# Performance work log

Measured on AMD Instinct MI355X. Metric: run time of the kernel, lower is better.

Reference implementation:

```python
import jax, jax.numpy as jnp
import numpy as np

E, EDIM, NDIM, H = 262144, 256, 256, 8
DH = NDIM // H
EPS = 1e-5  # torch nn.LayerNorm default


def _param(k, shape, scale=0.02):
    return jax.random.normal(k, shape, jnp.float32) * scale


def setup_inputs() -> dict:
    key = jax.random.key(0)
    ks = jax.random.split(key, 12)
    return {
        "x": jax.random.normal(ks[0], (E, EDIM), jnp.float32),
        "src_x": jax.random.normal(ks[1], (E, NDIM), jnp.float32),
        "dst_x": jax.random.normal(ks[2], (E, NDIM), jnp.float32),
        # multi-head cross-attention params (q from edge feats, k/v from node feats)
        "Wq": _param(ks[3], (EDIM, NDIM)), "bq": jnp.zeros((NDIM,), jnp.float32),
        "Wk": _param(ks[4], (NDIM, NDIM)), "bk": jnp.zeros((NDIM,), jnp.float32),
        "Wv": _param(ks[5], (NDIM, NDIM)), "bv": jnp.zeros((NDIM,), jnp.float32),
        "Wo": _param(ks[6], (NDIM, EDIM)), "bo": jnp.zeros((EDIM,), jnp.float32),
        "W1": _param(ks[7], (EDIM, 4 * EDIM)), "b1": jnp.zeros((4 * EDIM,), jnp.float32),
        "W2": _param(ks[8], (4 * EDIM, EDIM)), "b2": jnp.zeros((EDIM,), jnp.float32),
        # two LayerNorms
        "g1": jnp.ones((EDIM,), jnp.float32), "be1": jnp.zeros((EDIM,), jnp.float32),
        "g2": jnp.ones((EDIM,), jnp.float32), "be2": jnp.zeros((EDIM,), jnp.float32),
    }


def _layer_norm(h, g, b):
    m = jnp.mean(h, axis=-1, keepdims=True)
    v = jnp.mean(jnp.square(h - m), axis=-1, keepdims=True)
    return (h - m) * jax.lax.rsqrt(v + EPS) * g + b


def reference(x, src_x, dst_x, Wq, bq, Wk, bk, Wv, bv, Wo, bo,
              W1, b1, W2, b2, g1, be1, g2, be2):
    # per-edge cross-attention: query = edge feat (len 1), keys/values = (src, dst) (len 2)
    q = (x @ Wq + bq).reshape(E, H, DH)                 # [E,H,DH]
    kv = jnp.stack([src_x, dst_x], axis=1)              # [E,2,NDIM]
    k = (kv @ Wk + bk).reshape(E, 2, H, DH)
    v = (kv @ Wv + bv).reshape(E, 2, H, DH)
    scale = 1.0 / float(np.sqrt(DH))
    scores = jnp.einsum('ehd,ekhd->ehk', q, k) * scale  # [E,H,2]
    attn = jax.nn.softmax(scores, axis=-1)
    ctx = jnp.einsum('ehk,ekhd->ehd', attn, v).reshape(E, NDIM)
    out = ctx @ Wo + bo                                  # [E,EDIM]
    h = _layer_norm(x + out, g1, be1)
    ff = jax.nn.relu(h @ W1 + b1) @ W2 + b2
    return _layer_norm(h + ff, g2, be2)
```

## Files before the change

kernel.cpp:

```cpp
#include <hip/hip_runtime.h>
#include <hip/hip_bf16.h>
#include <math.h>

#define NROWS   262144
#define ABM     64
#define FBM     128
#define ATHR    256
#define FTHR    512
#define LDSB_A  (32768 + 32768 + 2048 + 512)
#define LDSB_B  (65536 + 65536)

using bf16x8 = __attribute__((ext_vector_type(8))) short;
using s16x4  = __attribute__((ext_vector_type(4))) short;
using f32x4  = __attribute__((ext_vector_type(4))) float;

__device__ __forceinline__ short f2bf(float f) {
  __hip_bfloat16 h = __float2bfloat16(f);
  return __builtin_bit_cast(short, h);
}
__device__ __forceinline__ float bf2f(short s) {
  __hip_bfloat16 h = __builtin_bit_cast(__hip_bfloat16, s);
  return __bfloat162float(h);
}
__device__ __forceinline__ unsigned pack2(float a, float b) {
  return (unsigned)(unsigned short)f2bf(a) | ((unsigned)(unsigned short)f2bf(b) << 16);
}
template <int RSTR>
__device__ __forceinline__ int swzR(int row, int col) {
  return row * RSTR + ((col * 2) ^ ((row & 7) << 4));
}
__device__ __forceinline__ int swz(int row, int col) {
  return swzR<512>(row, col);
}

__device__ __forceinline__ float red16(float p) {
  p += __shfl_xor(p, 1, 64);
  p += __shfl_xor(p, 2, 64);
  p += __shfl_xor(p, 4, 64);
  p += __shfl_xor(p, 8, 64);
  return p;
}

template <int MF, int NF, int KLEN = 256, int RSTR = 512>
__device__ __forceinline__ void gemmA(const char* __restrict__ Abuf,
                                      const short* __restrict__ WT, int Kw,
                                      int col0, int koff, int li, int hi,
                                      f32x4 (&acc)[MF][NF]) {
  const short* wp[NF];
#pragma unroll
  for (int n = 0; n < NF; ++n)
    wp[n] = WT + (size_t)(col0 + 16 * n + li) * Kw + koff + hi * 8;
#pragma unroll 2
  for (int kk = 0; kk < KLEN; kk += 32) {
    int ka = kk + hi * 8;
    bf16x8 b[NF];
#pragma unroll
    for (int n = 0; n < NF; ++n) b[n] = *(const bf16x8*)(wp[n] + kk);
    bf16x8 a[MF];
#pragma unroll
    for (int m = 0; m < MF; ++m)
      a[m] = *(const bf16x8*)(Abuf + swzR<RSTR>(16 * m + li, ka));
#pragma unroll
    for (int m = 0; m < MF; ++m)
#pragma unroll
      for (int n = 0; n < NF; ++n)
        acc[m][n] = __builtin_amdgcn_mfma_f32_16x16x32_bf16(a[m], b[n], acc[m][n], 0, 0, 0);
  }
}

template <int MF, int NF, int KLEN = 256, int RSTR = 512>
__device__ __forceinline__ void gemmF(const char* __restrict__ Abuf,
                                      const short* __restrict__ WT, int Kw,
                                      int col0, int koff, int li, int hi,
                                      f32x4 (&acc)[MF][NF]) {
  const short* wp[NF];
#pragma unroll
  for (int n = 0; n < NF; ++n)
    wp[n] = WT + (size_t)(col0 + 16 * n + li) * Kw + koff + hi * 8;
#pragma unroll 2
  for (int kk = 0; kk < KLEN; kk += 32) {
    int ka = kk + hi * 8;
    bf16x8 b[NF];
#pragma unroll
    for (int n = 0; n < NF; ++n) b[n] = *(const bf16x8*)(wp[n] + kk);
    bf16x8 a[MF];
#pragma unroll
    for (int m = 0; m < MF; ++m)
      a[m] = *(const bf16x8*)(Abuf + swzR<RSTR>(16 * m + li, ka));
#pragma unroll
    for (int m = 0; m < MF; ++m)
#pragma unroll
      for (int n = 0; n < NF; ++n)
        acc[m][n] = __builtin_amdgcn_mfma_f32_16x16x32_bf16(a[m], b[n], acc[m][n], 0, 0, 0);
  }
}

__device__ __forceinline__ void stage8(float4 (&ld)[8],
                                       const float* __restrict__ g,
                                       int tid, int half) {
#pragma unroll
  for (int it = 0; it < 8; ++it) {
    int idx = (half * 8 + it) * ATHR + tid;
    ld[it] = *(const float4*)(g + (idx >> 6) * 256 + ((idx & 63) << 2));
  }
}
__device__ __forceinline__ void write8(float4 (&ld)[8],
                                       char* __restrict__ buf,
                                       int tid, int half) {
#pragma unroll
  for (int it = 0; it < 8; ++it) {
    int idx = (half * 8 + it) * ATHR + tid;
    int r = idx >> 6, c = (idx & 63) << 2;
    s16x4 o;
    o[0] = f2bf(ld[it].x); o[1] = f2bf(ld[it].y);
    o[2] = f2bf(ld[it].z); o[3] = f2bf(ld[it].w);
    *(s16x4*)(buf + swz(r, c)) = o;
  }
}

__global__ void prep(const float* __restrict__ Wq, const float* __restrict__ Wk,
                     const float* __restrict__ Wv, const float* __restrict__ Wo,
                     const float* __restrict__ W1, const float* __restrict__ W2,
                     short* __restrict__ wt) {
  int idx = blockIdx.x * blockDim.x + threadIdx.x;
  if (idx < 262144) {
    int m = idx >> 16;
    const float* W = (m == 0) ? Wq : (m == 1) ? Wk : (m == 2) ? Wv : Wo;
    float s = (m == 0) ? 0.17677669529663687f : 1.0f;
    int l = idx & 65535;
    int n = l >> 8, k = l & 255;
    wt[idx] = f2bf(W[k * 256 + n] * s);
  } else if (idx < 524288) {
    int l = idx - 262144;
    int n = l >> 8, k = l & 255;
    wt[idx] = f2bf(W1[k * 1024 + n]);
  } else {
    int l = idx - 524288;
    int n = l >> 10, k = l & 1023;
    wt[idx] = f2bf(W2[k * 256 + n]);
  }
}

__global__ __launch_bounds__(ATHR, 2)
void attn_ln1(const float* __restrict__ x, const float* __restrict__ sx,
              const float* __restrict__ dx,
              const float* __restrict__ bq, const float* __restrict__ bv,
              const float* __restrict__ bo,
              const float* __restrict__ g1, const float* __restrict__ be1,
              const short* __restrict__ wt, short* __restrict__ hout) {
  extern __shared__ char sm[];
  char*  Cbuf = sm;
  char*  Tbuf = sm + 32768;
  float* sc   = (float*)(sm + 65536);
  float* scrM = (float*)(sm + 67584);

  const short* WqT = wt;
  const short* WkT = wt + 65536;
  const short* WvT = wt + 131072;
  const short* WoT = wt + 196608;

  const int tid  = threadIdx.x;
  const int w    = tid >> 6;
  const int lane = tid & 63;
  const int li   = lane & 15;
  const int hi   = lane >> 4;
  const int cw   = w * 64;
  const size_t row0 = (size_t)blockIdx.x * ABM;

  const float* xt = x  + row0 * 256;
  const float* st = sx + row0 * 256;
  const float* dt = dx + row0 * 256;

  float4 ld[8];

  stage8(ld, xt, tid, 0);
  write8(ld, Cbuf, tid, 0);
  stage8(ld, xt, tid, 1);
  write8(ld, Cbuf, tid, 1);
  __syncthreads();

  unsigned qb[4][4][2];
  {
    f32x4 qa[4][4];
#pragma unroll
    for (int m = 0; m < 4; ++m)
#pragma unroll
      for (int n = 0; n < 4; ++n) qa[m][n] = (f32x4){0.f, 0.f, 0.f, 0.f};
    stage8(ld, dt, tid, 0);
    gemmA<4, 4, 128>(Cbuf, WqT, 256, cw, 0, li, hi, qa);
    write8(ld, Tbuf, tid, 0);
    stage8(ld, dt, tid, 1);
    gemmA<4, 4, 128>(Cbuf + 256, WqT, 256, cw, 128, li, hi, qa);
    write8(ld, Tbuf, tid, 1);
    const float scl = 0.17677669529663687f;
#pragma unroll
    for (int n = 0; n < 4; ++n) {
      float bqn = bq[cw + 16 * n + li] * scl;
#pragma unroll
      for (int m = 0; m < 4; ++m) {
        qb[m][n][0] = pack2(qa[m][n][0] + bqn, qa[m][n][1] + bqn);
        qb[m][n][1] = pack2(qa[m][n][2] + bqn, qa[m][n][3] + bqn);
      }
    }
  }
  __syncthreads();

#define QF(m, n, j) bf2f((short)(((j) & 1) ? (qb[m][n][(j) >> 1] >> 16) \
                                           : (qb[m][n][(j) >> 1] & 0xffffu)))

  f32x4 vd[4][4];
  {
    stage8(ld, st, tid, 0);
#pragma unroll
    for (int hh = 0; hh < 2; ++hh) {
      f32x4 ka[4][2];
#pragma unroll
      for (int m = 0; m < 4; ++m)
#pragma unroll
        for (int n = 0; n < 2; ++n) ka[m][n] = (f32x4){0.f, 0.f, 0.f, 0.f};
      gemmA<4, 2>(Tbuf, WkT, 256, cw + 32 * hh, 0, li, hi, ka);
#pragma unroll
      for (int m = 0; m < 4; ++m)
#pragma unroll
        for (int j = 0; j < 4; ++j) {
          float pr = red16(QF(m, 2 * hh, j) * ka[m][0][j] +
                           QF(m, 2 * hh + 1, j) * ka[m][1][j]);
          if (li == 0) sc[(w * 2 + hh) * 64 + 16 * m + 4 * hi + j] = pr;
        }
    }
#pragma unroll
    for (int m = 0; m < 4; ++m)
#pragma unroll
      for (int n = 0; n < 4; ++n) vd[m][n] = (f32x4){0.f, 0.f, 0.f, 0.f};
    gemmA<4, 4>(Tbuf, WvT, 256, cw, 0, li, hi, vd);
  }
  __syncthreads();
  write8(ld, Tbuf, tid, 0);
  stage8(ld, st, tid, 1);
  write8(ld, Tbuf, tid, 1);
  __syncthreads();

#pragma unroll
  for (int hh = 0; hh < 2; ++hh) {
    f32x4 ka[4][2];
#pragma unroll
    for (int m = 0; m < 4; ++m)
#pragma unroll
      for (int n = 0; n < 2; ++n) ka[m][n] = (f32x4){0.f, 0.f, 0.f, 0.f};
    gemmA<4, 2>(Tbuf, WkT, 256, cw + 32 * hh, 0, li, hi, ka);
#pragma unroll
    for (int m = 0; m < 4; ++m)
#pragma unroll
      for (int j = 0; j < 4; ++j) {
        float ps = red16(QF(m, 2 * hh, j) * ka[m][0][j] +
                         QF(m, 2 * hh + 1, j) * ka[m][1][j]);
        int r = 16 * m + 4 * hi + j;
        float pdv = sc[(w * 2 + hh) * 64 + r];
        float awv = 1.f / (1.f + expf(pdv - ps));
        if (li == 0) sc[(w * 2 + hh) * 64 + r] = awv;
      }
  }
  {
    f32x4 vs[4][4];
#pragma unroll
    for (int m = 0; m < 4; ++m)
#pragma unroll
      for (int n = 0; n < 4; ++n) vs[m][n] = (f32x4){0.f, 0.f, 0.f, 0.f};
    gemmA<4, 4>(Tbuf, WvT, 256, cw, 0, li, hi, vs);
#pragma unroll
    for (int hh = 0; hh < 2; ++hh)
#pragma unroll
      for (int n2 = 0; n2 < 2; ++n2) {
        int n = 2 * hh + n2;
        float bvn = bv[cw + 16 * n + li];
#pragma unroll
        for (int m = 0; m < 4; ++m)
#pragma unroll
          for (int j = 0; j < 4; ++j) {
            float a = sc[(w * 2 + hh) * 64 + 16 * m + 4 * hi + j];
            vs[m][n][j] = a * vs[m][n][j] + (1.f - a) * vd[m][n][j] + bvn;
          }
      }
    __syncthreads();
#pragma unroll
    for (int m = 0; m < 4; ++m)
#pragma unroll
      for (int n = 0; n < 4; ++n)
#pragma unroll
        for (int j = 0; j < 4; ++j)
          *(short*)(Tbuf + swz(16 * m + 4 * hi + j, cw + 16 * n + li)) = f2bf(vs[m][n][j]);
  }
  __syncthreads();

  {
    f32x4 oa[4][4];
#pragma unroll
    for (int m = 0; m < 4; ++m)
#pragma unroll
      for (int n = 0; n < 4; ++n) oa[m][n] = (f32x4){0.f, 0.f, 0.f, 0.f};
    gemmA<4, 4>(Tbuf, WoT, 256, cw, 0, li, hi, oa);
#pragma unroll
    for (int n = 0; n < 4; ++n) {
      float bon = bo[cw + 16 * n + li];
#pragma unroll
      for (int m = 0; m < 4; ++m)
#pragma unroll
        for (int j = 0; j < 4; ++j) {
          int r = 16 * m + 4 * hi + j;
          float xv = bf2f(*(short*)(Cbuf + swz(r, cw + 16 * n + li)));
          oa[m][n][j] += bon + xv;
        }
    }
#pragma unroll
    for (int m = 0; m < 4; ++m)
#pragma unroll
      for (int j = 0; j < 4; ++j) {
        int r = 16 * m + 4 * hi + j;
        float sv = oa[m][0][j] + oa[m][1][j] + oa[m][2][j] + oa[m][3][j];
        float qv = oa[m][0][j] * oa[m][0][j] + oa[m][1][j] * oa[m][1][j]
                 + oa[m][2][j] * oa[m][2][j] + oa[m][3][j] * oa[m][3][j];
        float s = red16(sv);
        float q = red16(qv);
        if (li == 0) { sc[(w * 64 + r) * 2] = s; sc[(w * 64 + r) * 2 + 1] = q; }
      }
    __syncthreads();
    if (tid < ABM) {
      float S = 0.f, Q = 0.f;
#pragma unroll
      for (int ww = 0; ww < 4; ++ww) {
        S += sc[(ww * 64 + tid) * 2];
        Q += sc[(ww * 64 + tid) * 2 + 1];
      }
      float mean = S * (1.f / 256.f);
      float var  = Q * (1.f / 256.f) - mean * mean;
      scrM[tid * 2] = mean;
      scrM[tid * 2 + 1] = rsqrtf(var + 1e-5f);
    }
    __syncthreads();
#pragma unroll
    for (int n = 0; n < 4; ++n) {
      float g1n = g1[cw + 16 * n + li];
      float b1n = be1[cw + 16 * n + li];
#pragma unroll
      for (int m = 0; m < 4; ++m)
#pragma unroll
        for (int j = 0; j < 4; ++j) {
          int r = 16 * m + 4 * hi + j;
          float mean = scrM[r * 2], rs = scrM[r * 2 + 1];
          *(short*)(Cbuf + swz(r, cw + 16 * n + li)) =
              f2bf((oa[m][n][j] - mean) * rs * g1n + b1n);
        }
    }
  }
  __syncthreads();

  {
    short* hrow = hout + row0 * 256;
#pragma unroll
    for (int t = 0; t < 8; ++t) {
      int idx = t * ATHR + tid;
      int r = idx >> 5, c16 = idx & 31;
      bf16x8 v = *(bf16x8*)(Cbuf + r * 512 + ((c16 * 16) ^ ((r & 7) << 4)));
      *(bf16x8*)(hrow + r * 256 + c16 * 8) = v;
    }
  }
#undef QF
}

__global__ __launch_bounds__(FTHR, 2)
void ffn_ln2(const short* __restrict__ hin, const float* __restrict__ b1,
             const float* __restrict__ b2,
             const float* __restrict__ g2, const float* __restrict__ be2,
             const short* __restrict__ wt, float* __restrict__ out) {
  extern __shared__ char sm[];
  char* Cbuf = sm;
  char* Hbuf = sm + 65536;
  float* scrP = (float*)Hbuf;
  float* scrM = (float*)(Hbuf + 8192);

  const short* W1T = wt + 262144;
  const short* W2T = wt + 524288;

  const int tid  = threadIdx.x;
  const int w    = tid >> 6;
  const int lane = tid & 63;
  const int li   = lane & 15;
  const int hi   = lane >> 4;
  const int cw   = w * 32;
  const size_t row0 = (size_t)blockIdx.x * FBM;

  {
    const short* hrow = hin + row0 * 256;
#pragma unroll
    for (int t = 0; t < 8; ++t) {
      int idx = t * FTHR + tid;
      int r = idx >> 5, c16 = idx & 31;
      bf16x8 v = *(const bf16x8*)(hrow + r * 256 + c16 * 8);
      *(bf16x8*)(Cbuf + r * 512 + ((c16 * 16) ^ ((r & 7) << 4))) = v;
    }
  }
  __syncthreads();

  f32x4 a2[8][2];
#pragma unroll
  for (int m = 0; m < 8; ++m)
#pragma unroll
    for (int n = 0; n < 2; ++n) a2[m][n] = (f32x4){0.f, 0.f, 0.f, 0.f};
#pragma unroll 1
  for (int c = 0; c < 4; ++c) {
#pragma unroll
    for (int nf = 0; nf < 2; ++nf) {
      f32x4 a1[8][1];
#pragma unroll
      for (int m = 0; m < 8; ++m) a1[m][0] = (f32x4){0.f, 0.f, 0.f, 0.f};
      gemmF<8, 1, 256, 512>(Cbuf, W1T, 256, 256 * c + cw + 16 * nf, 0, li, hi, a1);
      float b1n = b1[256 * c + cw + 16 * nf + li];
      int lc = cw + 16 * nf + li;
#pragma unroll
      for (int m = 0; m < 8; ++m)
#pragma unroll
        for (int j = 0; j < 4; ++j) {
          int r = 16 * m + 4 * hi + j;
          *(short*)(Hbuf + swzR<512>(r, lc)) = f2bf(fmaxf(a1[m][0][j] + b1n, 0.f));
        }
    }
    __syncthreads();
    gemmF<8, 2, 256, 512>(Hbuf, W2T, 1024, cw, 256 * c, li, hi, a2);
    __syncthreads();
  }

  {
#pragma unroll
    for (int n = 0; n < 2; ++n) {
      float b2n = b2[cw + 16 * n + li];
#pragma unroll
      for (int m = 0; m < 8; ++m)
#pragma unroll
        for (int j = 0; j < 4; ++j) {
          int r = 16 * m + 4 * hi + j;
          a2[m][n][j] += b2n + bf2f(*(short*)(Cbuf + swz(r, cw + 16 * n + li)));
        }
    }
  }
  __syncthreads();

#pragma unroll
  for (int m = 0; m < 8; ++m)
#pragma unroll
    for (int j = 0; j < 4; ++j) {
      int r = 16 * m + 4 * hi + j;
      float sv = a2[m][0][j] + a2[m][1][j];
      float qv = a2[m][0][j] * a2[m][0][j] + a2[m][1][j] * a2[m][1][j];
      float s = red16(sv);
      float q = red16(qv);
      if (li == 0) { scrP[(w * 128 + r) * 2] = s; scrP[(w * 128 + r) * 2 + 1] = q; }
    }
  __syncthreads();
  if (tid < FBM) {
    float S = 0.f, Q = 0.f;
#pragma unroll
    for (int ww = 0; ww < 8; ++ww) {
      S += scrP[(ww * 128 + tid) * 2];
      Q += scrP[(ww * 128 + tid) * 2 + 1];
    }
    float mean = S * (1.f / 256.f);
    float var  = Q * (1.f / 256.f) - mean * mean;
    scrM[tid * 2] = mean;
    scrM[tid * 2 + 1] = rsqrtf(var + 1e-5f);
  }
  __syncthreads();

  {
    float g2n[2], b2n[2];
#pragma unroll
    for (int n = 0; n < 2; ++n) {
      g2n[n] = g2[cw + 16 * n + li];
      b2n[n] = be2[cw + 16 * n + li];
    }
    float* orow = out + row0 * 256;
#pragma unroll
    for (int hf = 0; hf < 4; ++hf) {
#pragma unroll
      for (int m2 = 0; m2 < 2; ++m2) {
        int m = 2 * hf + m2;
#pragma unroll
        for (int n = 0; n < 2; ++n)
#pragma unroll
          for (int j = 0; j < 4; ++j) {
            int r = 16 * m + 4 * hi + j;
            float mean = scrM[r * 2], rs = scrM[r * 2 + 1];
            int rr = r - 32 * hf;
            *(float*)(Cbuf + rr * 1024 + (((cw + 16 * n + li) * 4) ^ ((rr & 7) << 4)))
                = (a2[m][n][j] - mean) * rs * g2n[n] + b2n[n];
          }
      }
      __syncthreads();
#pragma unroll
      for (int t = 0; t < 4; ++t) {
        int idx = t * FTHR + tid;
        int r = idx >> 6, c4 = idx & 63;
        f32x4 v = *(f32x4*)(Cbuf + r * 1024 + ((c4 * 16) ^ ((r & 7) << 4)));
        *(f32x4*)(orow + (hf * 32 + r) * 256 + c4 * 4) = v;
      }
      __syncthreads();
    }
  }
}

extern "C" void kernel_launch(void* const* d_in, const int* in_sizes, int n_in,
                              void* d_out, int out_size, void* d_ws, size_t ws_size,
                              hipStream_t stream) {
  const float* x   = (const float*)d_in[0];
  const float* sx  = (const float*)d_in[1];
  const float* dx  = (const float*)d_in[2];
  const float* Wq  = (const float*)d_in[3];
  const float* bq  = (const float*)d_in[4];
  const float* Wk  = (const float*)d_in[5];
  const float* Wv  = (const float*)d_in[7];
  const float* bv  = (const float*)d_in[8];
  const float* Wo  = (const float*)d_in[9];
  const float* bo  = (const float*)d_in[10];
  const float* W1  = (const float*)d_in[11];
  const float* b1  = (const float*)d_in[12];
  const float* W2  = (const float*)d_in[13];
  const float* b2  = (const float*)d_in[14];
  const float* g1  = (const float*)d_in[15];
  const float* be1 = (const float*)d_in[16];
  const float* g2  = (const float*)d_in[17];
  const float* be2 = (const float*)d_in[18];
  short* wt = (short*)d_ws;
  short* hbuf = wt + 786432;

  prep<<<dim3(1536), dim3(512), 0, stream>>>(Wq, Wk, Wv, Wo, W1, W2, wt);
  attn_ln1<<<dim3(NROWS / ABM), dim3(ATHR), LDSB_A, stream>>>(
      x, sx, dx, bq, bv, bo, g1, be1, wt, hbuf);
  ffn_ln2<<<dim3(NROWS / FBM), dim3(FTHR), LDSB_B, stream>>>(
      hbuf, b1, b2, g2, be2, wt, (float*)d_out);
}
```

Baseline: 1.075 ms.

## Double FFN block threads to 1024 with 16 waves each owning 16 columns

The FFN+LayerNorm kernel now launches 1024 threads per block instead of 512, so each of 16 waves owns a 16-column slice rather than 32. Per-thread accumulators halve, and the load, LN partial-sum and store loops are resized to match. The aim is more waves in flight to hide memory and MFMA latency. The cost is that each wave reloads the full A-operand from LDS for narrower outputs, LDS traffic per MFMA doubles, the LN reduction gets twice as many partials, and block-wide barriers cover more waves.

```diff
diff --git a/kernel.cpp b/kernel.cpp
--- a/kernel.cpp
+++ b/kernel.cpp
@@ -6,7 +6,7 @@
 #define ABM     64
 #define FBM     128
 #define ATHR    256
-#define FTHR    512
+#define FTHR    1024
 #define LDSB_A  (32768 + 32768 + 2048 + 512)
 #define LDSB_B  (65536 + 65536)
 
@@ -367,7 +367,7 @@
 #undef QF
 }
 
-__global__ __launch_bounds__(FTHR, 2)
+__global__ __launch_bounds__(FTHR, 4)
 void ffn_ln2(const short* __restrict__ hin, const float* __restrict__ b1,
              const float* __restrict__ b2,
              const float* __restrict__ g2, const float* __restrict__ be2,
@@ -376,7 +376,7 @@
   char* Cbuf = sm;
   char* Hbuf = sm + 65536;
   float* scrP = (float*)Hbuf;
-  float* scrM = (float*)(Hbuf + 8192);
+  float* scrM = (float*)(Hbuf + 16384);
 
   const short* W1T = wt + 262144;
   const short* W2T = wt + 524288;
@@ -386,13 +386,13 @@
   const int lane = tid & 63;
   const int li   = lane & 15;
   const int hi   = lane >> 4;
-  const int cw   = w * 32;
+  const int cw   = w * 16;
   const size_t row0 = (size_t)blockIdx.x * FBM;
 
   {
     const short* hrow = hin + row0 * 256;
 #pragma unroll
-    for (int t = 0; t < 8; ++t) {
+    for (int t = 0; t < 4; ++t) {
       int idx = t * FTHR + tid;
       int r = idx >> 5, c16 = idx & 31;
       bf16x8 v = *(const bf16x8*)(hrow + r * 256 + c16 * 8);
@@ -401,21 +401,18 @@
   }
   __syncthreads();
 
-  f32x4 a2[8][2];
-#pragma unroll
-  for (int m = 0; m < 8; ++m)
-#pragma unroll
-    for (int n = 0; n < 2; ++n) a2[m][n] = (f32x4){0.f, 0.f, 0.f, 0.f};
+  f32x4 a2[8][1];
+#pragma unroll
+  for (int m = 0; m < 8; ++m) a2[m][0] = (f32x4){0.f, 0.f, 0.f, 0.f};
 #pragma unroll 1
   for (int c = 0; c < 4; ++c) {
-#pragma unroll
-    for (int nf = 0; nf < 2; ++nf) {
-      f32x4 a1[8][1];
-#pragma unroll
-      for (int m = 0; m < 8; ++m) a1[m][0] = (f32x4){0.f, 0.f, 0.f, 0.f};
-      gemmF<8, 1, 256, 512>(Cbuf, W1T, 256, 256 * c + cw + 16 * nf, 0, li, hi, a1);
-      float b1n = b1[256 * c + cw + 16 * nf + li];
-      int lc = cw + 16 * nf + li;
+    f32x4 a1[8][1];
+#pragma unroll
+    for (int m = 0; m < 8; ++m) a1[m][0] = (f32x4){0.f, 0.f, 0.f, 0.f};
+    gemmF<8, 1, 256, 512>(Cbuf, W1T, 256, 256 * c + cw, 0, li, hi, a1);
+    {
+      float b1n = b1[256 * c + cw + li];
+      int lc = cw + li;
 #pragma unroll
       for (int m = 0; m < 8; ++m)
 #pragma unroll
@@ -425,22 +422,19 @@
         }
     }
     __syncthreads();
-    gemmF<8, 2, 256, 512>(Hbuf, W2T, 1024, cw, 256 * c, li, hi, a2);
+    gemmF<8, 1, 256, 512>(Hbuf, W2T, 1024, cw, 256 * c, li, hi, a2);
     __syncthreads();
   }
 
   {
-#pragma unroll
-    for (int n = 0; n < 2; ++n) {
-      float b2n = b2[cw + 16 * n + li];
-#pragma unroll
-      for (int m = 0; m < 8; ++m)
-#pragma unroll
-        for (int j = 0; j < 4; ++j) {
-          int r = 16 * m + 4 * hi + j;
-          a2[m][n][j] += b2n + bf2f(*(short*)(Cbuf + swz(r, cw + 16 * n + li)));
-        }
-    }
+    float b2n = b2[cw + li];
+#pragma unroll
+    for (int m = 0; m < 8; ++m)
+#pragma unroll
+      for (int j = 0; j < 4; ++j) {
+        int r = 16 * m + 4 * hi + j;
+        a2[m][0][j] += b2n + bf2f(*(short*)(Cbuf + swz(r, cw + li)));
+      }
   }
   __syncthreads();
 
@@ -449,17 +443,15 @@
 #pragma unroll
     for (int j = 0; j < 4; ++j) {
       int r = 16 * m + 4 * hi + j;
-      float sv = a2[m][0][j] + a2[m][1][j];
-      float qv = a2[m][0][j] * a2[m][0][j] + a2[m][1][j] * a2[m][1][j];
-      float s = red16(sv);
-      float q = red16(qv);
+      float s = red16(a2[m][0][j]);
+      float q = red16(a2[m][0][j] * a2[m][0][j]);
       if (li == 0) { scrP[(w * 128 + r) * 2] = s; scrP[(w * 128 + r) * 2 + 1] = q; }
     }
   __syncthreads();
   if (tid < FBM) {
     float S = 0.f, Q = 0.f;
 #pragma unroll
-    for (int ww = 0; ww < 8; ++ww) {
+    for (int ww = 0; ww < 16; ++ww) {
       S += scrP[(ww * 128 + tid) * 2];
       Q += scrP[(ww * 128 + tid) * 2 + 1];
     }
@@ -471,12 +463,8 @@
   __syncthreads();
 
   {
-    float g2n[2], b2n[2];
-#pragma unroll
-    for (int n = 0; n < 2; ++n) {
-      g2n[n] = g2[cw + 16 * n + li];
-      b2n[n] = be2[cw + 16 * n + li];
-    }
+    float g2n = g2[cw + li];
+    float b2n = be2[cw + li];
     float* orow = out + row0 * 256;
 #pragma unroll
     for (int hf = 0; hf < 4; ++hf) {
@@ -484,19 +472,17 @@
       for (int m2 = 0; m2 < 2; ++m2) {
         int m = 2 * hf + m2;
 #pragma unroll
-        for (int n = 0; n < 2; ++n)
-#pragma unroll
-          for (int j = 0; j < 4; ++j) {
-            int r = 16 * m + 4 * hi + j;
-            float mean = scrM[r * 2], rs = scrM[r * 2 + 1];
-            int rr = r - 32 * hf;
-            *(float*)(Cbuf + rr * 1024 + (((cw + 16 * n + li) * 4) ^ ((rr & 7) << 4)))
-                = (a2[m][n][j] - mean) * rs * g2n[n] + b2n[n];
-          }
+        for (int j = 0; j < 4; ++j) {
+          int r = 16 * m + 4 * hi + j;
+          float mean = scrM[r * 2], rs = scrM[r * 2 + 1];
+          int rr = r - 32 * hf;
+          *(float*)(Cbuf + rr * 1024 + (((cw + li) * 4) ^ ((rr & 7) << 4)))
+              = (a2[m][0][j] - mean) * rs * g2n + b2n;
+        }
       }
       __syncthreads();
 #pragma unroll
-      for (int t = 0; t < 4; ++t) {
+      for (int t = 0; t < 2; ++t) {
         int idx = t * FTHR + tid;
         int r = idx >> 6, c4 = idx & 63;
         f32x4 v = *(f32x4*)(Cbuf + r * 1024 + ((c4 * 16) ^ ((r & 7) << 4)));
```

After: 1.175 ms. 1.09x slower.
